# Kernel optimization log

Hardware: AMD Instinct MI355X
Metric: run time of the kernel (lower is better)

## Reference

```python
import jax, jax.numpy as jnp
import numpy as np


def _local_patches(x, patch_size):
    """Zero-padded sliding patches, matching F.unfold semantics.
    x: [N, C, H, W] -> [N, C, P*P, H, W] (window positions row-major,
    same per-channel ordering as unfold's C*P*P channel layout)."""
    N, C, H, W = x.shape
    pad = patch_size // 2
    xp = jnp.pad(x, ((0, 0), (0, 0), (pad, pad), (pad, pad)))
    views = [xp[:, :, i:i + H, j:j + W]
             for i in range(patch_size) for j in range(patch_size)]
    return jnp.stack(views, axis=2)  # [N, C, P*P, H, W]


def setup_inputs() -> dict:
    key = jax.random.key(0)
    x_lab = jax.random.normal(key, (16, 3, 512, 512), dtype=jnp.float32)
    return {"x_lab": x_lab, "patch_size": 3, "alpha": 1, "scale_factor": 1}


def reference(x_lab, patch_size, alpha, scale_factor):
    # scale_factor == 1 -> F.interpolate is the identity (nearest, scale 1).
    patches = _local_patches(x_lab, patch_size)       # [N, 3, P*P, H, W]
    local_l = patches[:, 0]                            # [N, P*P, H, W]
    local_a = patches[:, 1]
    local_b = patches[:, 2]
    l = x_lab[:, 0:1]                                  # [N, 1, H, W]
    local_difference = (local_l - l) ** 2
    correlation = jax.nn.softmax(-local_difference / alpha, axis=1)
    wa = jnp.sum(correlation * local_a, axis=1, keepdims=True)
    wb = jnp.sum(correlation * local_b, axis=1, keepdims=True)
    return jnp.concatenate([wa, wb], axis=1)           # [N, 2, H, W]
```

## Files before the change

kernel.cpp:

```cpp
#include <hip/hip_runtime.h>

#define NB   16
#define HH   512
#define WW   512
#define HWSZ (HH * WW)

typedef float vfloat4 __attribute__((ext_vector_type(4)));

__device__ __forceinline__ void load_row6(const float* __restrict__ p, int base,
                                          bool rowv, bool ledge, bool redge,
                                          float v[6]) {
    vfloat4 c = (vfloat4){0.f, 0.f, 0.f, 0.f};
    float lw = 0.0f, rx = 0.0f;
    if (rowv) {
        c = *(const vfloat4*)(p + base);
        if (!ledge) lw = p[base - 1];
        if (!redge) rx = p[base + 4];
    }
    v[0] = lw; v[1] = c.x; v[2] = c.y; v[3] = c.z; v[4] = c.w; v[5] = rx;
}

__global__ __launch_bounds__(256) void WeightedAverage_kernel(
    const float* __restrict__ x,
    const int*   __restrict__ alpha_p,
    float*       __restrict__ out)
{
    int g   = blockIdx.x * 256 + threadIdx.x;
    int col = (g & 127) << 2;
    int h   = (g >> 7) & 511;
    int n   = g >> 16;
    bool ledge = (col == 0);
    bool redge = (col + 4 == WW);

    float m = -1.4426950408889634f / (float)(*alpha_p);

    const float* Lp = x + (size_t)n * 3 * HWSZ;
    const float* Ap = Lp + HWSZ;
    const float* Bp = Lp + 2 * HWSZ;

    float Lr[3][6];
    int  rb[3];
    bool rv[3];
#pragma unroll
    for (int i = 0; i < 3; ++i) {
        int r = h - 1 + i;
        rv[i] = ((unsigned)r < (unsigned)HH);
        rb[i] = r * WW + col;
        load_row6(Lp, rb[i], rv[i], ledge, redge, Lr[i]);
    }

    float l[4] = { Lr[1][1], Lr[1][2], Lr[1][3], Lr[1][4] };
    float den[4] = {0.f,0.f,0.f,0.f};
    float na[4]  = {0.f,0.f,0.f,0.f};
    float nb[4]  = {0.f,0.f,0.f,0.f};

#pragma unroll
    for (int i = 0; i < 3; ++i) {
        float Ar[6], Br[6];
        load_row6(Ap, rb[i], rv[i], ledge, redge, Ar);
        load_row6(Bp, rb[i], rv[i], ledge, redge, Br);
#pragma unroll
        for (int dx = 0; dx < 3; ++dx) {
#pragma unroll
            for (int j = 0; j < 4; ++j) {
                float d  = Lr[i][j + dx] - l[j];
                float wt = (i == 1 && dx == 1) ? 1.0f : exp2f(d * d * m);
                den[j] += wt;
                na[j]  += wt * Ar[j + dx];
                nb[j]  += wt * Br[j + dx];
            }
        }
    }

    float r0 = __builtin_amdgcn_rcpf(den[0]);
    float r1 = __builtin_amdgcn_rcpf(den[1]);
    float r2 = __builtin_amdgcn_rcpf(den[2]);
    float r3 = __builtin_amdgcn_rcpf(den[3]);
    vfloat4 oa = (vfloat4){na[0]*r0, na[1]*r1, na[2]*r2, na[3]*r3};
    vfloat4 ob = (vfloat4){nb[0]*r0, nb[1]*r1, nb[2]*r2, nb[3]*r3};

    float* op = out + (size_t)n * 2 * HWSZ + (size_t)h * WW + col;
    __builtin_nontemporal_store(oa, (vfloat4*)op);
    __builtin_nontemporal_store(ob, (vfloat4*)(op + HWSZ));
}

extern "C" void kernel_launch(void* const* d_in, const int* in_sizes, int n_in,
                              void* d_out, int out_size, void* d_ws, size_t ws_size,
                              hipStream_t stream) {
    const float* x     = (const float*)d_in[0];
    const int*   alpha = (const int*)d_in[2];
    float*       out   = (float*)d_out;

    int groups = NB * HWSZ / 4;
    dim3 grid(groups / 256);
    WeightedAverage_kernel<<<grid, 256, 0, stream>>>(x, alpha, out);
}
```

Baseline: 107.3 us.

## Compute a 4x4 output tile per thread to reuse loaded neighbor rows

Each thread now computes four consecutive output rows of four columns instead of one row, loading six input rows of L/A/B once and reusing them across the overlapping 3x3 windows. This reduces redundant global/cache loads of halo rows. The grid shrinks fourfold and register pressure rises (48 accumulators plus 36 L values), which lowers occupancy and latency hiding.

Result: faster. 101.8 us (-5.2%).

```diff
diff --git a/kernel.cpp b/kernel.cpp
--- a/kernel.cpp
+++ b/kernel.cpp
@@ -27,8 +27,8 @@
 {
     int g   = blockIdx.x * 256 + threadIdx.x;
     int col = (g & 127) << 2;
-    int h   = (g >> 7) & 511;
-    int n   = g >> 16;
+    int h0  = ((g >> 7) & 127) << 2;
+    int n   = g >> 14;
     bool ledge = (col == 0);
     bool redge = (col + 4 == WW);
 
@@ -38,50 +38,58 @@
     const float* Ap = Lp + HWSZ;
     const float* Bp = Lp + 2 * HWSZ;
 
-    float Lr[3][6];
-    int  rb[3];
-    bool rv[3];
+    float Lr[6][6];
+    int  rb[6];
+    bool rv[6];
 #pragma unroll
-    for (int i = 0; i < 3; ++i) {
-        int r = h - 1 + i;
-        rv[i] = ((unsigned)r < (unsigned)HH);
-        rb[i] = r * WW + col;
-        load_row6(Lp, rb[i], rv[i], ledge, redge, Lr[i]);
+    for (int s = 0; s < 6; ++s) {
+        int r = h0 - 1 + s;
+        rv[s] = ((unsigned)r < (unsigned)HH);
+        rb[s] = r * WW + col;
+        load_row6(Lp, rb[s], rv[s], ledge, redge, Lr[s]);
     }
 
-    float l[4] = { Lr[1][1], Lr[1][2], Lr[1][3], Lr[1][4] };
-    float den[4] = {0.f,0.f,0.f,0.f};
-    float na[4]  = {0.f,0.f,0.f,0.f};
-    float nb[4]  = {0.f,0.f,0.f,0.f};
+    float den[4][4], na[4][4], nb[4][4];
+#pragma unroll
+    for (int i = 0; i < 4; ++i)
+#pragma unroll
+        for (int j = 0; j < 4; ++j) { den[i][j] = 0.f; na[i][j] = 0.f; nb[i][j] = 0.f; }
 
 #pragma unroll
-    for (int i = 0; i < 3; ++i) {
+    for (int s = 0; s < 6; ++s) {
         float Ar[6], Br[6];
-        load_row6(Ap, rb[i], rv[i], ledge, redge, Ar);
-        load_row6(Bp, rb[i], rv[i], ledge, redge, Br);
+        load_row6(Ap, rb[s], rv[s], ledge, redge, Ar);
+        load_row6(Bp, rb[s], rv[s], ledge, redge, Br);
+        const int ilo = (s - 2 < 0) ? 0 : s - 2;
+        const int ihi = (s < 3) ? s : 3;
 #pragma unroll
-        for (int dx = 0; dx < 3; ++dx) {
+        for (int i = ilo; i <= ihi; ++i) {
 #pragma unroll
-            for (int j = 0; j < 4; ++j) {
-                float d  = Lr[i][j + dx] - l[j];
-                float wt = (i == 1 && dx == 1) ? 1.0f : exp2f(d * d * m);
-                den[j] += wt;
-                na[j]  += wt * Ar[j + dx];
-                nb[j]  += wt * Br[j + dx];
+            for (int dx = 0; dx < 3; ++dx) {
+#pragma unroll
+                for (int j = 0; j < 4; ++j) {
+                    float d  = Lr[s][j + dx] - Lr[i + 1][j + 1];
+                    float wt = (s == i + 1 && dx == 1) ? 1.0f : exp2f(d * d * m);
+                    den[i][j] += wt;
+                    na[i][j]  += wt * Ar[j + dx];
+                    nb[i][j]  += wt * Br[j + dx];
+                }
             }
         }
     }
 
-    float r0 = __builtin_amdgcn_rcpf(den[0]);
-    float r1 = __builtin_amdgcn_rcpf(den[1]);
-    float r2 = __builtin_amdgcn_rcpf(den[2]);
-    float r3 = __builtin_amdgcn_rcpf(den[3]);
-    vfloat4 oa = (vfloat4){na[0]*r0, na[1]*r1, na[2]*r2, na[3]*r3};
-    vfloat4 ob = (vfloat4){nb[0]*r0, nb[1]*r1, nb[2]*r2, nb[3]*r3};
-
-    float* op = out + (size_t)n * 2 * HWSZ + (size_t)h * WW + col;
-    __builtin_nontemporal_store(oa, (vfloat4*)op);
-    __builtin_nontemporal_store(ob, (vfloat4*)(op + HWSZ));
+    float* op = out + (size_t)n * 2 * HWSZ + (size_t)h0 * WW + col;
+#pragma unroll
+    for (int i = 0; i < 4; ++i) {
+        float r0 = __builtin_amdgcn_rcpf(den[i][0]);
+        float r1 = __builtin_amdgcn_rcpf(den[i][1]);
+        float r2 = __builtin_amdgcn_rcpf(den[i][2]);
+        float r3 = __builtin_amdgcn_rcpf(den[i][3]);
+        vfloat4 oa = (vfloat4){na[i][0]*r0, na[i][1]*r1, na[i][2]*r2, na[i][3]*r3};
+        vfloat4 ob = (vfloat4){nb[i][0]*r0, nb[i][1]*r1, nb[i][2]*r2, nb[i][3]*r3};
+        __builtin_nontemporal_store(oa, (vfloat4*)(op + (size_t)i * WW));
+        __builtin_nontemporal_store(ob, (vfloat4*)(op + (size_t)i * WW + HWSZ));
+    }
 }
 
 extern "C" void kernel_launch(void* const* d_in, const int* in_sizes, int n_in,
@@ -91,7 +99,7 @@
     const int*   alpha = (const int*)d_in[2];
     float*       out   = (float*)d_out;
 
-    int groups = NB * HWSZ / 4;
-    dim3 grid(groups / 256);
+    int threads = NB * (HH / 4) * (WW / 4);
+    dim3 grid(threads / 256);
     WeightedAverage_kernel<<<grid, 256, 0, stream>>>(x, alpha, out);
 }
```
